# Optimization experiments

Measured on AMD Instinct MI355X. Metric: run time of the kernel, lower is better.

## Reference

```python
import jax, jax.numpy as jnp
import numpy as np


def setup_inputs() -> dict:
    key = jax.random.key(0)
    k1, k2 = jax.random.split(key)
    E, T, N = 65536, 4096, 10000
    edge_index = jax.random.randint(k1, (2, E), 0, N)
    # target edges are a subset of edge_index columns so every target exists
    target_edges = edge_index[:, :T]
    score = jax.random.normal(k2, (E,), dtype=jnp.float32)
    return {
        "edge_index": edge_index,
        "score": score,
        "target_edges": target_edges,
        "num_nodes": N,
    }


def reference(edge_index, score, target_edges, num_nodes):
    # Vectorized form of the per-target-edge loop:
    # for each target edge (s, d):
    #   mask_e      = (src_e == s) | (dst_e == d)
    #   CE over score[mask] with target = position of the exact edge (s, d)
    #   contribution = CE / K  where K = mask.sum()
    src, dst = edge_index[0], edge_index[1]            # [E]
    t_src, t_dst = target_edges[0], target_edges[1]    # [T]

    same_src = src[None, :] == t_src[:, None]          # [T, E]
    same_dst = dst[None, :] == t_dst[:, None]          # [T, E]
    mask = same_src | same_dst                         # candidate set per target
    is_tgt = same_src & same_dst                       # exact target edge hits

    exists = jnp.any(is_tgt, axis=1)                   # [T]
    K = jnp.sum(mask, axis=1).astype(score.dtype)      # [T] ragged subset sizes

    NEG = jnp.asarray(-1e30, score.dtype)
    masked_logits = jnp.where(mask, score[None, :], NEG)   # [T, E]
    lse = jax.nn.logsumexp(masked_logits, axis=1)           # [T]

    # argmax over bool picks the FIRST matching edge, matching torch argmax(-1)
    tgt_idx = jnp.argmax(is_tgt, axis=1)                # [T]
    tgt_logit = score[tgt_idx]                          # [T]

    # cross_entropy = lse - target_logit; divided by subset size K
    loss_t = jnp.where(exists, (lse - tgt_logit) / K, 0.0)
    return jnp.sum(loss_t) / target_edges.shape[1]
```

## Files before the change

### kernel.cpp

```cpp
#include <hip/hip_runtime.h>
#include <hip/hip_bf16.h>
#include <stdint.h>


#define HLOG 13
#define HSZ  (1u << HLOG)
#define NCAP 16384
#define NBW  (NCAP / 32)
#define EMPTY64 0xFFFFFFFFFFFFFFFFull
#define M40     ((1ull << 40) - 1)
#define CNT1    (1ull << 40)
#define FSCALE      4194304.0f
#define INV_FSCALE  (1.0f / 4194304.0f)

typedef unsigned long long u64;
typedef unsigned int u32;

__device__ __forceinline__ u32 hash64(u64 k) {
    return (u32)((k * 0x9E3779B97F4A7C15ull) >> (64 - HLOG));
}

#define FF_BYTES   ((size_t)HSZ * 8 + (size_t)HSZ * 4)
#define Z_BYTES    ((size_t)HSZ * 8 + 2 * (size_t)NCAP * 8 + 2 * (size_t)NBW * 4 + 8)

__global__ __launch_bounds__(256) void la_init(u64* __restrict__ p,
                                               int n_ff, int n_tot)
{
    int i = blockIdx.x * 256 + threadIdx.x;
    const int stride = gridDim.x * 256;
    for (; i < n_tot; i += stride)
        p[i] = (i < n_ff) ? EMPTY64 : 0ull;
}

__global__ __launch_bounds__(256) void la_insert(
    const int* __restrict__ tsrc, const int* __restrict__ tdst,
    u64* __restrict__ hkey, u32* __restrict__ sbit, u32* __restrict__ dbit,
    int T)
{
    const int t = blockIdx.x * 256 + threadIdx.x;
    if (t >= T) return;
    const u32 a = (u32)tsrc[t], b = (u32)tdst[t];
    if (a < NCAP) atomicOr(&sbit[a >> 5], 1u << (a & 31));
    if (b < NCAP) atomicOr(&dbit[b >> 5], 1u << (b & 31));
    const u64 key = ((u64)a << 32) | b;
    u32 h = hash64(key);
    while (true) {
        const u64 prev = atomicCAS(&hkey[h], EMPTY64, key);
        if (prev == EMPTY64 || prev == key) break;
        h = (h + 1) & (HSZ - 1);
    }
}

__global__ __launch_bounds__(256) void la_edges(
    const int* __restrict__ src, const int* __restrict__ dst,
    const float* __restrict__ score,
    const u64* __restrict__ hkey, u64* __restrict__ hpack,
    u32* __restrict__ hmin,
    u64* __restrict__ nodeS, u64* __restrict__ nodeD,
    const u32* __restrict__ sbit, const u32* __restrict__ dbit, int E)
{
    const int e = blockIdx.x * 256 + threadIdx.x;
    if (e >= E) return;
    const u32 s = (u32)src[e], d = (u32)dst[e];
    if (s >= NCAP || d >= NCAP) return;

    const bool hs = (sbit[s >> 5] >> (s & 31)) & 1u;
    const bool hd = (dbit[d >> 5] >> (d & 31)) & 1u;
    if (!hs && !hd) return;

    const float ev = __expf(score[e]);
    const u64 add = (u64)(ev * FSCALE + 0.5f) + CNT1;

    if (hs) atomicAdd(&nodeS[s], add);
    if (hd) atomicAdd(&nodeD[d], add);

    if (hs && hd) {
        const u64 key = ((u64)s << 32) | d;
        u32 h = hash64(key);
        while (true) {
            const u64 k2 = hkey[h];
            if (k2 == EMPTY64) break;
            if (k2 == key) {
                atomicAdd(&hpack[h], add);
                atomicMin(&hmin[h], (u32)e);
                break;
            }
            h = (h + 1) & (HSZ - 1);
        }
    }
}

__global__ __launch_bounds__(64) void la_targets(
    const int* __restrict__ tsrc, const int* __restrict__ tdst,
    const float* __restrict__ score,
    const u64* __restrict__ hkey, const u64* __restrict__ hpack,
    const u32* __restrict__ hmin,
    const u64* __restrict__ nodeS, const u64* __restrict__ nodeD,
    float* __restrict__ partial, u32* __restrict__ done,
    float* __restrict__ out, int T)
{
    const int nb = gridDim.x;
    const int t  = blockIdx.x * 64 + threadIdx.x;
    float local = 0.0f;
    if (t < T) {
        const u32 a = (u32)tsrc[t], b = (u32)tdst[t];
        const u64 key = ((u64)a << 32) | b;
        u32 h = hash64(key);
        int slot = -1;
        while (true) {
            const u64 k2 = hkey[h];
            if (k2 == key) { slot = (int)h; break; }
            if (k2 == EMPTY64) break;
            h = (h + 1) & (HSZ - 1);
        }
        if (slot >= 0) {
            const u64 pk = hpack[slot];
            const u64 cb = pk >> 40;
            if (cb > 0) {
                const u64 pa = nodeS[a], pb = nodeD[b];
                const u64 Sfix = (pa & M40) + (pb & M40) - (pk & M40);
                const u64 Kc   = (pa >> 40) + (pb >> 40) - cb;
                const float S  = (float)Sfix * INV_FSCALE;
                local = (logf(S) - score[hmin[slot]]) / (float)Kc;
            }
        }
    }
    for (int off = 32; off > 0; off >>= 1) local += __shfl_down(local, off);

    __shared__ int lastFlag;
    if (threadIdx.x == 0) {
        __hip_atomic_store(&partial[blockIdx.x], local, __ATOMIC_RELEASE,
                           __HIP_MEMORY_SCOPE_AGENT);
        const u32 prev = __hip_atomic_fetch_add(done, 1u, __ATOMIC_ACQ_REL,
                                                __HIP_MEMORY_SCOPE_AGENT);
        lastFlag = (prev == (u32)(nb - 1));
    }
    __syncthreads();

    if (lastFlag) {
        float s = 0.0f;
        for (int i = threadIdx.x; i < nb; i += 64)
            s += __hip_atomic_load(&partial[i], __ATOMIC_RELAXED,
                                   __HIP_MEMORY_SCOPE_AGENT);
        for (int off = 32; off > 0; off >>= 1) s += __shfl_down(s, off);
        if (threadIdx.x == 0) out[0] = s / (float)T;
    }
}

#define NT   8
#define BLK  256

__global__ __launch_bounds__(BLK) void la_loss_main(
    const int* __restrict__ src, const int* __restrict__ dst,
    const float* __restrict__ score,
    const int* __restrict__ tsrc, const int* __restrict__ tdst,
    float* __restrict__ partial, int E, int T)
{
    const int tid   = threadIdx.x;
    const int tbase = blockIdx.x * NT;
    if (tbase >= T) return;

    int ts[NT], td[NT];
#pragma unroll
    for (int j = 0; j < NT; ++j) {
        int tj = tbase + j; if (tj > T - 1) tj = T - 1;
        ts[j] = tsrc[tj];
        td[j] = tdst[tj];
    }

    float S[NT]; float Kc[NT]; int idx[NT];
#pragma unroll
    for (int j = 0; j < NT; ++j) { S[j] = 0.0f; Kc[j] = 0.0f; idx[j] = 0x7fffffff; }

    for (int it = tid * 4; it < E; it += BLK * 4) {
        const int4   vs = *reinterpret_cast<const int4*>(src + it);
        const int4   vd = *reinterpret_cast<const int4*>(dst + it);
        const float4 sc = *reinterpret_cast<const float4*>(score + it);
        const int   es[4] = { vs.x, vs.y, vs.z, vs.w };
        const int   ed[4] = { vd.x, vd.y, vd.z, vd.w };
        const float ev[4] = { __expf(sc.x), __expf(sc.y), __expf(sc.z), __expf(sc.w) };
#pragma unroll
        for (int j = 0; j < NT; ++j) {
#pragma unroll
            for (int k = 0; k < 4; ++k) {
                const bool ms = (es[k] == ts[j]);
                const bool md = (ed[k] == td[j]);
                const bool m  = ms | md;
                S[j]  += m ? ev[k] : 0.0f;
                Kc[j] += m ? 1.0f  : 0.0f;
                idx[j] = (ms & md) ? min(idx[j], it + k) : idx[j];
            }
        }
    }

#pragma unroll
    for (int j = 0; j < NT; ++j) {
        for (int off = 32; off > 0; off >>= 1) {
            S[j]  += __shfl_down(S[j],  off);
            Kc[j] += __shfl_down(Kc[j], off);
            idx[j] = min(idx[j], __shfl_down(idx[j], off));
        }
    }

    __shared__ float sS[4][NT];
    __shared__ float sK[4][NT];
    __shared__ int   sI[4][NT];
    const int wave = tid >> 6;
    const int lane = tid & 63;
    if (lane == 0) {
#pragma unroll
        for (int j = 0; j < NT; ++j) { sS[wave][j] = S[j]; sK[wave][j] = Kc[j]; sI[wave][j] = idx[j]; }
    }
    __syncthreads();

    if (tid < NT && (tbase + tid) < T) {
        float Ssum = 0.0f, Ksum = 0.0f;
        int im = 0x7fffffff;
#pragma unroll
        for (int w = 0; w < 4; ++w) {
            Ssum += sS[w][tid]; Ksum += sK[w][tid]; im = min(im, sI[w][tid]);
        }
        float loss = 0.0f;
        if (im != 0x7fffffff) loss = (logf(Ssum) - score[im]) / Ksum;
        partial[tbase + tid] = loss;
    }
}

__global__ __launch_bounds__(256) void la_loss_reduce(
    const float* __restrict__ partial, float* __restrict__ out, int T)
{
    float s = 0.0f;
    for (int i = threadIdx.x; i < T; i += 256) s += partial[i];
    for (int off = 32; off > 0; off >>= 1) s += __shfl_down(s, off);
    __shared__ float acc[4];
    if ((threadIdx.x & 63) == 0) acc[threadIdx.x >> 6] = s;
    __syncthreads();
    if (threadIdx.x == 0) out[0] = (acc[0] + acc[1] + acc[2] + acc[3]) / (float)T;
}


extern "C" void kernel_launch(void* const* d_in, const int* in_sizes, int n_in,
                              void* d_out, int out_size, void* d_ws, size_t ws_size,
                              hipStream_t stream) {
    const int*   edge_index = (const int*)d_in[0];
    const float* score      = (const float*)d_in[1];
    const int*   target     = (const int*)d_in[2];

    const int E = in_sizes[0] / 2;
    const int T = in_sizes[2] / 2;

    const int* src  = edge_index;
    const int* dst  = edge_index + E;
    const int* tsrc = target;
    const int* tdst = target + T;

    const int    nb   = (T + 63) / 64;
    const size_t need = FF_BYTES + Z_BYTES + (size_t)nb * 4;

    if (ws_size >= need) {
        uint8_t* p = (uint8_t*)d_ws;
        u64* hkey  = (u64*)p;                          p += (size_t)HSZ * 8;
        u32* hmin  = (u32*)p;                          p += (size_t)HSZ * 4;
        u64* hpack = (u64*)p;                          p += (size_t)HSZ * 8;
        u64* nodeS = (u64*)p;                          p += (size_t)NCAP * 8;
        u64* nodeD = (u64*)p;                          p += (size_t)NCAP * 8;
        u32* sbit  = (u32*)p;                          p += (size_t)NBW * 4;
        u32* dbit  = (u32*)p;                          p += (size_t)NBW * 4;
        u32* done  = (u32*)p;                          p += 8;
        float* partial = (float*)p;

        const int n_ff  = (int)(FF_BYTES / 8);
        const int n_tot = (int)((FF_BYTES + Z_BYTES) / 8);

        la_init<<<64, 256, 0, stream>>>((u64*)d_ws, n_ff, n_tot);
        la_insert<<<(T + 255) / 256, 256, 0, stream>>>(tsrc, tdst, hkey,
                                                       sbit, dbit, T);
        la_edges<<<(E + 255) / 256, 256, 0, stream>>>(src, dst, score, hkey,
                                                      hpack, hmin, nodeS, nodeD,
                                                      sbit, dbit, E);
        la_targets<<<nb, 64, 0, stream>>>(tsrc, tdst, score, hkey, hpack, hmin,
                                          nodeS, nodeD, partial, done,
                                          (float*)d_out, T);
    } else {
        float* partial = (float*)d_ws;
        la_loss_main<<<(T + NT - 1) / NT, BLK, 0, stream>>>(src, dst, score,
                                                            tsrc, tdst, partial, E, T);
        la_loss_reduce<<<1, 256, 0, stream>>>(partial, (float*)d_out, T);
    }
}
```

Before: 33.45 us.

## Fuse hash pipeline into one persistent kernel with grid barriers

```diff
diff --git a/kernel.cpp b/kernel.cpp
--- a/kernel.cpp
+++ b/kernel.cpp
@@ -7,12 +7,15 @@
 #define HSZ  (1u << HLOG)
 #define NCAP 16384
 #define NBW  (NCAP / 32)
-#define EMPTY64 0xFFFFFFFFFFFFFFFFull
 #define M40     ((1ull << 40) - 1)
 #define CNT1    (1ull << 40)
 #define FSCALE      4194304.0f
 #define INV_FSCALE  (1.0f / 4194304.0f)
 
+#define NBLK 128
+#define TPB  512
+#define NTH  (NBLK * TPB)
+
 typedef unsigned long long u64;
 typedef unsigned int u32;
 
@@ -20,97 +23,87 @@
     return (u32)((k * 0x9E3779B97F4A7C15ull) >> (64 - HLOG));
 }
 
-#define FF_BYTES   ((size_t)HSZ * 8 + (size_t)HSZ * 4)
-#define Z_BYTES    ((size_t)HSZ * 8 + 2 * (size_t)NCAP * 8 + 2 * (size_t)NBW * 4 + 8)
-
-__global__ __launch_bounds__(256) void la_init(u64* __restrict__ p,
-                                               int n_ff, int n_tot)
-{
-    int i = blockIdx.x * 256 + threadIdx.x;
-    const int stride = gridDim.x * 256;
-    for (; i < n_tot; i += stride)
-        p[i] = (i < n_ff) ? EMPTY64 : 0ull;
-}
-
-__global__ __launch_bounds__(256) void la_insert(
-    const int* __restrict__ tsrc, const int* __restrict__ tdst,
-    u64* __restrict__ hkey, u32* __restrict__ sbit, u32* __restrict__ dbit,
-    int T)
-{
-    const int t = blockIdx.x * 256 + threadIdx.x;
-    if (t >= T) return;
-    const u32 a = (u32)tsrc[t], b = (u32)tdst[t];
-    if (a < NCAP) atomicOr(&sbit[a >> 5], 1u << (a & 31));
-    if (b < NCAP) atomicOr(&dbit[b >> 5], 1u << (b & 31));
-    const u64 key = ((u64)a << 32) | b;
-    u32 h = hash64(key);
-    while (true) {
-        const u64 prev = atomicCAS(&hkey[h], EMPTY64, key);
-        if (prev == EMPTY64 || prev == key) break;
-        h = (h + 1) & (HSZ - 1);
-    }
-}
-
-__global__ __launch_bounds__(256) void la_edges(
+__device__ __forceinline__ void gbar(u32* bar, int phase, int nblk) {
+    __syncthreads();
+    if (threadIdx.x == 0) {
+        const u32 prev = __hip_atomic_fetch_add(&bar[1 + phase], 1u,
+                                                __ATOMIC_ACQ_REL,
+                                                __HIP_MEMORY_SCOPE_AGENT);
+        if (prev == (u32)(nblk - 1)) {
+            __hip_atomic_store(&bar[0], (u32)(phase + 1), __ATOMIC_RELEASE,
+                               __HIP_MEMORY_SCOPE_AGENT);
+        } else {
+            while (__hip_atomic_load(&bar[0], __ATOMIC_ACQUIRE,
+                                     __HIP_MEMORY_SCOPE_AGENT) <= (u32)phase) {}
+        }
+    }
+    __syncthreads();
+}
+
+__global__ __launch_bounds__(TPB) void la_onekernel(
     const int* __restrict__ src, const int* __restrict__ dst,
     const float* __restrict__ score,
-    const u64* __restrict__ hkey, u64* __restrict__ hpack,
-    u32* __restrict__ hmin,
+    const int* __restrict__ tsrc, const int* __restrict__ tdst,
+    u64* __restrict__ hkey, u64* __restrict__ hpack,
     u64* __restrict__ nodeS, u64* __restrict__ nodeD,
-    const u32* __restrict__ sbit, const u32* __restrict__ dbit, int E)
+    u32* __restrict__ hmax, u32* __restrict__ sbit, u32* __restrict__ dbit,
+    u32* __restrict__ bar, float* __restrict__ wpart,
+    float* __restrict__ out, int E, int T)
 {
-    const int e = blockIdx.x * 256 + threadIdx.x;
-    if (e >= E) return;
-    const u32 s = (u32)src[e], d = (u32)dst[e];
-    if (s >= NCAP || d >= NCAP) return;
-
-    const bool hs = (sbit[s >> 5] >> (s & 31)) & 1u;
-    const bool hd = (dbit[d >> 5] >> (d & 31)) & 1u;
-    if (!hs && !hd) return;
-
-    const float ev = __expf(score[e]);
-    const u64 add = (u64)(ev * FSCALE + 0.5f) + CNT1;
-
-    if (hs) atomicAdd(&nodeS[s], add);
-    if (hd) atomicAdd(&nodeD[d], add);
-
-    if (hs && hd) {
-        const u64 key = ((u64)s << 32) | d;
+    const int gtid = blockIdx.x * TPB + threadIdx.x;
+    const int nblk = gridDim.x;
+
+    for (int t = gtid; t < T; t += NTH) {
+        const u32 a = (u32)tsrc[t], b = (u32)tdst[t];
+        if (a < NCAP) atomicOr(&sbit[a >> 5], 1u << (a & 31));
+        if (b < NCAP) atomicOr(&dbit[b >> 5], 1u << (b & 31));
+        const u64 key = ((u64)(a + 1) << 32) | b;
         u32 h = hash64(key);
         while (true) {
-            const u64 k2 = hkey[h];
-            if (k2 == EMPTY64) break;
-            if (k2 == key) {
-                atomicAdd(&hpack[h], add);
-                atomicMin(&hmin[h], (u32)e);
-                break;
+            const u64 prev = atomicCAS(&hkey[h], 0ull, key);
+            if (prev == 0ull || prev == key) break;
+            h = (h + 1) & (HSZ - 1);
+        }
+    }
+    gbar(bar, 0, nblk);
+
+    for (int e = gtid; e < E; e += NTH) {
+        const u32 s = (u32)src[e], d = (u32)dst[e];
+        const float sc = score[e];
+        const bool hs = (s < NCAP) && ((sbit[s >> 5] >> (s & 31)) & 1u);
+        const bool hd = (d < NCAP) && ((dbit[d >> 5] >> (d & 31)) & 1u);
+        if (hs | hd) {
+            const u64 add = (u64)(__expf(sc) * FSCALE + 0.5f) + CNT1;
+            if (hs) atomicAdd(&nodeS[s], add);
+            if (hd) atomicAdd(&nodeD[d], add);
+            if (hs & hd) {
+                const u64 key = ((u64)(s + 1) << 32) | d;
+                u32 h = hash64(key);
+                while (true) {
+                    const u64 k2 = hkey[h];
+                    if (k2 == 0ull) break;
+                    if (k2 == key) {
+                        atomicAdd(&hpack[h], add);
+                        atomicMax(&hmax[h], ~(u32)e);
+                        break;
+                    }
+                    h = (h + 1) & (HSZ - 1);
+                }
             }
-            h = (h + 1) & (HSZ - 1);
-        }
-    }
-}
-
-__global__ __launch_bounds__(64) void la_targets(
-    const int* __restrict__ tsrc, const int* __restrict__ tdst,
-    const float* __restrict__ score,
-    const u64* __restrict__ hkey, const u64* __restrict__ hpack,
-    const u32* __restrict__ hmin,
-    const u64* __restrict__ nodeS, const u64* __restrict__ nodeD,
-    float* __restrict__ partial, u32* __restrict__ done,
-    float* __restrict__ out, int T)
-{
-    const int nb = gridDim.x;
-    const int t  = blockIdx.x * 64 + threadIdx.x;
+        }
+    }
+    gbar(bar, 1, nblk);
+
     float local = 0.0f;
-    if (t < T) {
+    for (int t = gtid; t < T; t += NTH) {
         const u32 a = (u32)tsrc[t], b = (u32)tdst[t];
-        const u64 key = ((u64)a << 32) | b;
+        const u64 key = ((u64)(a + 1) << 32) | b;
         u32 h = hash64(key);
         int slot = -1;
         while (true) {
             const u64 k2 = hkey[h];
             if (k2 == key) { slot = (int)h; break; }
-            if (k2 == EMPTY64) break;
+            if (k2 == 0ull) break;
             h = (h + 1) & (HSZ - 1);
         }
         if (slot >= 0) {
@@ -120,30 +113,34 @@
                 const u64 pa = nodeS[a], pb = nodeD[b];
                 const u64 Sfix = (pa & M40) + (pb & M40) - (pk & M40);
                 const u64 Kc   = (pa >> 40) + (pb >> 40) - cb;
-                const float S  = (float)Sfix * INV_FSCALE;
-                local = (logf(S) - score[hmin[slot]]) / (float)Kc;
+                const int idx  = (int)(~hmax[slot]);
+                local += (logf((float)Sfix * INV_FSCALE) - score[idx])
+                         / (float)Kc;
             }
         }
     }
     for (int off = 32; off > 0; off >>= 1) local += __shfl_down(local, off);
 
-    __shared__ int lastFlag;
-    if (threadIdx.x == 0) {
-        __hip_atomic_store(&partial[blockIdx.x], local, __ATOMIC_RELEASE,
+    const int nw  = ((T + 63) / 64 < NTH / 64) ? (T + 63) / 64 : NTH / 64;
+    const int wid = gtid >> 6;
+    if ((threadIdx.x & 63) == 0 && wid < nw)
+        __hip_atomic_store(&wpart[wid], local, __ATOMIC_RELEASE,
                            __HIP_MEMORY_SCOPE_AGENT);
-        const u32 prev = __hip_atomic_fetch_add(done, 1u, __ATOMIC_ACQ_REL,
-                                                __HIP_MEMORY_SCOPE_AGENT);
-        lastFlag = (prev == (u32)(nb - 1));
-    }
-    __syncthreads();
-
-    if (lastFlag) {
-        float s = 0.0f;
-        for (int i = threadIdx.x; i < nb; i += 64)
-            s += __hip_atomic_load(&partial[i], __ATOMIC_RELAXED,
-                                   __HIP_MEMORY_SCOPE_AGENT);
-        for (int off = 32; off > 0; off >>= 1) s += __shfl_down(s, off);
-        if (threadIdx.x == 0) out[0] = s / (float)T;
+    gbar(bar, 2, nblk);
+
+    if (blockIdx.x == 0) {
+        float s2 = 0.0f;
+        for (int i = threadIdx.x; i < nw; i += TPB) s2 += wpart[i];
+        for (int off = 32; off > 0; off >>= 1) s2 += __shfl_down(s2, off);
+        __shared__ float acc[TPB / 64];
+        if ((threadIdx.x & 63) == 0) acc[threadIdx.x >> 6] = s2;
+        __syncthreads();
+        if (threadIdx.x == 0) {
+            float r = 0.0f;
+#pragma unroll
+            for (int w = 0; w < TPB / 64; ++w) r += acc[w];
+            out[0] = r / (float)T;
+        }
     }
 }
 
@@ -254,33 +251,28 @@
     const int* tsrc = target;
     const int* tdst = target + T;
 
-    const int    nb   = (T + 63) / 64;
-    const size_t need = FF_BYTES + Z_BYTES + (size_t)nb * 4;
+    const int nw = ((T + 63) / 64 < NTH / 64) ? (T + 63) / 64 : NTH / 64;
+    const size_t need = (size_t)HSZ * 8 * 2 + (size_t)NCAP * 8 * 2
+                      + (size_t)HSZ * 4 + 2 * (size_t)NBW * 4 + 32
+                      + (size_t)nw * 4;
 
     if (ws_size >= need) {
         uint8_t* p = (uint8_t*)d_ws;
         u64* hkey  = (u64*)p;                          p += (size_t)HSZ * 8;
-        u32* hmin  = (u32*)p;                          p += (size_t)HSZ * 4;
         u64* hpack = (u64*)p;                          p += (size_t)HSZ * 8;
         u64* nodeS = (u64*)p;                          p += (size_t)NCAP * 8;
         u64* nodeD = (u64*)p;                          p += (size_t)NCAP * 8;
+        u32* hmax  = (u32*)p;                          p += (size_t)HSZ * 4;
         u32* sbit  = (u32*)p;                          p += (size_t)NBW * 4;
         u32* dbit  = (u32*)p;                          p += (size_t)NBW * 4;
-        u32* done  = (u32*)p;                          p += 8;
-        float* partial = (float*)p;
-
-        const int n_ff  = (int)(FF_BYTES / 8);
-        const int n_tot = (int)((FF_BYTES + Z_BYTES) / 8);
-
-        la_init<<<64, 256, 0, stream>>>((u64*)d_ws, n_ff, n_tot);
-        la_insert<<<(T + 255) / 256, 256, 0, stream>>>(tsrc, tdst, hkey,
-                                                       sbit, dbit, T);
-        la_edges<<<(E + 255) / 256, 256, 0, stream>>>(src, dst, score, hkey,
-                                                      hpack, hmin, nodeS, nodeD,
-                                                      sbit, dbit, E);
-        la_targets<<<nb, 64, 0, stream>>>(tsrc, tdst, score, hkey, hpack, hmin,
-                                          nodeS, nodeD, partial, done,
-                                          (float*)d_out, T);
+        u32* bar   = (u32*)p;                          p += 32;
+        float* wpart = (float*)p;
+
+        hipMemsetAsync(d_ws, 0, need, stream);
+        la_onekernel<<<NBLK, TPB, 0, stream>>>(src, dst, score, tsrc, tdst,
+                                               hkey, hpack, nodeS, nodeD,
+                                               hmax, sbit, dbit, bar, wpart,
+                                               (float*)d_out, E, T);
     } else {
         float* partial = (float*)d_ws;
         la_loss_main<<<(T + NT - 1) / NT, BLK, 0, stream>>>(src, dst, score,
```

Result: slower. 84.07 us (+151.4%).

## Build target hash table per block in LDS and fuse insert with edge pass

Applied to the files above, without the earlier changes.

```diff
diff --git a/kernel.cpp b/kernel.cpp
--- a/kernel.cpp
+++ b/kernel.cpp
@@ -3,89 +3,120 @@
 #include <stdint.h>
 
 
+#define NCAP 16384
+#define NBW  (NCAP / 32)
 #define HLOG 13
 #define HSZ  (1u << HLOG)
-#define NCAP 16384
-#define NBW  (NCAP / 32)
-#define EMPTY64 0xFFFFFFFFFFFFFFFFull
 #define M40     ((1ull << 40) - 1)
 #define CNT1    (1ull << 40)
 #define FSCALE      4194304.0f
 #define INV_FSCALE  (1.0f / 4194304.0f)
 
+#define NBLK 128
+#define TPB  512
+
 typedef unsigned long long u64;
 typedef unsigned int u32;
 
-__device__ __forceinline__ u32 hash64(u64 k) {
-    return (u32)((k * 0x9E3779B97F4A7C15ull) >> (64 - HLOG));
-}
-
-#define FF_BYTES   ((size_t)HSZ * 8 + (size_t)HSZ * 4)
-#define Z_BYTES    ((size_t)HSZ * 8 + 2 * (size_t)NCAP * 8 + 2 * (size_t)NBW * 4 + 8)
-
-__global__ __launch_bounds__(256) void la_init(u64* __restrict__ p,
-                                               int n_ff, int n_tot)
-{
-    int i = blockIdx.x * 256 + threadIdx.x;
-    const int stride = gridDim.x * 256;
-    for (; i < n_tot; i += stride)
-        p[i] = (i < n_ff) ? EMPTY64 : 0ull;
-}
-
-__global__ __launch_bounds__(256) void la_insert(
-    const int* __restrict__ tsrc, const int* __restrict__ tdst,
-    u64* __restrict__ hkey, u32* __restrict__ sbit, u32* __restrict__ dbit,
-    int T)
-{
-    const int t = blockIdx.x * 256 + threadIdx.x;
-    if (t >= T) return;
-    const u32 a = (u32)tsrc[t], b = (u32)tdst[t];
-    if (a < NCAP) atomicOr(&sbit[a >> 5], 1u << (a & 31));
-    if (b < NCAP) atomicOr(&dbit[b >> 5], 1u << (b & 31));
-    const u64 key = ((u64)a << 32) | b;
-    u32 h = hash64(key);
+__device__ __forceinline__ u32 hash28(u32 k) {
+    return (k * 2654435761u) >> (32 - HLOG);
+}
+
+__device__ __forceinline__ void lds_min_u16(u32* word, int hi, u32 t) {
+    u32 old = *word;
     while (true) {
-        const u64 prev = atomicCAS(&hkey[h], EMPTY64, key);
-        if (prev == EMPTY64 || prev == key) break;
-        h = (h + 1) & (HSZ - 1);
-    }
-}
-
-__global__ __launch_bounds__(256) void la_edges(
+        const u32 cur = hi ? (old >> 16) : (old & 0xFFFFu);
+        if (t >= cur) break;
+        const u32 nw = hi ? ((old & 0x0000FFFFu) | (t << 16))
+                          : ((old & 0xFFFF0000u) | t);
+        const u32 prev = atomicCAS(word, old, nw);
+        if (prev == old) break;
+        old = prev;
+    }
+}
+
+__global__ __launch_bounds__(TPB) void la_merge(
     const int* __restrict__ src, const int* __restrict__ dst,
     const float* __restrict__ score,
-    const u64* __restrict__ hkey, u64* __restrict__ hpack,
-    u32* __restrict__ hmin,
+    const int* __restrict__ tsrc, const int* __restrict__ tdst,
     u64* __restrict__ nodeS, u64* __restrict__ nodeD,
-    const u32* __restrict__ sbit, const u32* __restrict__ dbit, int E)
+    u64* __restrict__ bothPack, u32* __restrict__ bothMax,
+    u32* __restrict__ canon, int E, int T)
 {
-    const int e = blockIdx.x * 256 + threadIdx.x;
-    if (e >= E) return;
-    const u32 s = (u32)src[e], d = (u32)dst[e];
-    if (s >= NCAP || d >= NCAP) return;
-
-    const bool hs = (sbit[s >> 5] >> (s & 31)) & 1u;
-    const bool hd = (dbit[d >> 5] >> (d & 31)) & 1u;
-    if (!hs && !hd) return;
-
-    const float ev = __expf(score[e]);
-    const u64 add = (u64)(ev * FSCALE + 0.5f) + CNT1;
-
-    if (hs) atomicAdd(&nodeS[s], add);
-    if (hd) atomicAdd(&nodeD[d], add);
-
-    if (hs && hd) {
-        const u64 key = ((u64)s << 32) | d;
-        u32 h = hash64(key);
+    __shared__ u32 keys[HSZ];
+    __shared__ u32 valw[HSZ / 2];
+    __shared__ u32 sbits[NBW];
+    __shared__ u32 dbits[NBW];
+
+    const int tid = threadIdx.x;
+
+    for (int i = tid; i < HSZ; i += TPB)      keys[i] = 0xFFFFFFFFu;
+    for (int i = tid; i < HSZ / 2; i += TPB)  valw[i] = 0xFFFFFFFFu;
+    for (int i = tid; i < NBW; i += TPB)    { sbits[i] = 0u; dbits[i] = 0u; }
+    __syncthreads();
+
+    for (int t = tid; t < T; t += TPB) {
+        const u32 a = (u32)tsrc[t], b = (u32)tdst[t];
+        if (a >= NCAP || b >= NCAP) continue;
+        atomicOr(&sbits[a >> 5], 1u << (a & 31));
+        atomicOr(&dbits[b >> 5], 1u << (b & 31));
+        const u32 key = a * (u32)NCAP + b;
+        u32 h = hash28(key);
         while (true) {
-            const u64 k2 = hkey[h];
-            if (k2 == EMPTY64) break;
-            if (k2 == key) {
-                atomicAdd(&hpack[h], add);
-                atomicMin(&hmin[h], (u32)e);
-                break;
+            const u32 prev = atomicCAS(&keys[h], 0xFFFFFFFFu, key);
+            if (prev == 0xFFFFFFFFu || prev == key) break;
+            h = (h + 1) & (HSZ - 1);
+        }
+        lds_min_u16(&valw[h >> 1], h & 1, (u32)t);
+    }
+    __syncthreads();
+
+    if (blockIdx.x == 0) {
+        for (int t = tid; t < T; t += TPB) {
+            const u32 a = (u32)tsrc[t], b = (u32)tdst[t];
+            u32 c = (u32)t;
+            if (a < NCAP && b < NCAP) {
+                const u32 key = a * (u32)NCAP + b;
+                u32 h = hash28(key);
+                while (true) {
+                    const u32 k2 = keys[h];
+                    if (k2 == key) {
+                        const u32 w = valw[h >> 1];
+                        c = (h & 1) ? (w >> 16) : (w & 0xFFFFu);
+                        break;
+                    }
+                    if (k2 == 0xFFFFFFFFu) break;
+                    h = (h + 1) & (HSZ - 1);
+                }
             }
-            h = (h + 1) & (HSZ - 1);
+            canon[t] = c;
+        }
+    }
+
+    for (int e = blockIdx.x * TPB + tid; e < E; e += NBLK * TPB) {
+        const u32 s = (u32)src[e], d = (u32)dst[e];
+        if (s >= NCAP || d >= NCAP) continue;
+        const bool hs = (sbits[s >> 5] >> (s & 31)) & 1u;
+        const bool hd = (dbits[d >> 5] >> (d & 31)) & 1u;
+        if (!(hs | hd)) continue;
+        const u64 add = (u64)(__expf(score[e]) * FSCALE + 0.5f) + CNT1;
+        if (hs) atomicAdd(&nodeS[s], add);
+        if (hd) atomicAdd(&nodeD[d], add);
+        if (hs & hd) {
+            const u32 key = s * (u32)NCAP + d;
+            u32 h = hash28(key);
+            while (true) {
+                const u32 k2 = keys[h];
+                if (k2 == 0xFFFFFFFFu) break;
+                if (k2 == key) {
+                    const u32 w = valw[h >> 1];
+                    const u32 c = (h & 1) ? (w >> 16) : (w & 0xFFFFu);
+                    atomicAdd(&bothPack[c], add);
+                    atomicMax(&bothMax[c], ~(u32)e);
+                    break;
+                }
+                h = (h + 1) & (HSZ - 1);
+            }
         }
     }
 }
@@ -93,9 +124,9 @@
 __global__ __launch_bounds__(64) void la_targets(
     const int* __restrict__ tsrc, const int* __restrict__ tdst,
     const float* __restrict__ score,
-    const u64* __restrict__ hkey, const u64* __restrict__ hpack,
-    const u32* __restrict__ hmin,
     const u64* __restrict__ nodeS, const u64* __restrict__ nodeD,
+    const u64* __restrict__ bothPack, const u32* __restrict__ bothMax,
+    const u32* __restrict__ canon,
     float* __restrict__ partial, u32* __restrict__ done,
     float* __restrict__ out, int T)
 {
@@ -104,24 +135,17 @@
     float local = 0.0f;
     if (t < T) {
         const u32 a = (u32)tsrc[t], b = (u32)tdst[t];
-        const u64 key = ((u64)a << 32) | b;
-        u32 h = hash64(key);
-        int slot = -1;
-        while (true) {
-            const u64 k2 = hkey[h];
-            if (k2 == key) { slot = (int)h; break; }
-            if (k2 == EMPTY64) break;
-            h = (h + 1) & (HSZ - 1);
-        }
-        if (slot >= 0) {
-            const u64 pk = hpack[slot];
+        if (a < NCAP && b < NCAP) {
+            const u32 c  = canon[t];
+            const u64 pk = bothPack[c];
             const u64 cb = pk >> 40;
             if (cb > 0) {
                 const u64 pa = nodeS[a], pb = nodeD[b];
                 const u64 Sfix = (pa & M40) + (pb & M40) - (pk & M40);
                 const u64 Kc   = (pa >> 40) + (pb >> 40) - cb;
-                const float S  = (float)Sfix * INV_FSCALE;
-                local = (logf(S) - score[hmin[slot]]) / (float)Kc;
+                const int idx  = (int)(~bothMax[c]);
+                local = (logf((float)Sfix * INV_FSCALE) - score[idx])
+                        / (float)Kc;
             }
         }
     }
@@ -254,33 +278,27 @@
     const int* tsrc = target;
     const int* tdst = target + T;
 
-    const int    nb   = (T + 63) / 64;
-    const size_t need = FF_BYTES + Z_BYTES + (size_t)nb * 4;
-
-    if (ws_size >= need) {
+    const int nb = (T + 63) / 64;
+    const size_t need = 2 * (size_t)NCAP * 8 + (size_t)T * 8
+                      + 2 * (size_t)T * 4 + 32 + (size_t)nb * 4;
+
+    if (ws_size >= need && T < 65536) {
         uint8_t* p = (uint8_t*)d_ws;
-        u64* hkey  = (u64*)p;                          p += (size_t)HSZ * 8;
-        u32* hmin  = (u32*)p;                          p += (size_t)HSZ * 4;
-        u64* hpack = (u64*)p;                          p += (size_t)HSZ * 8;
-        u64* nodeS = (u64*)p;                          p += (size_t)NCAP * 8;
-        u64* nodeD = (u64*)p;                          p += (size_t)NCAP * 8;
-        u32* sbit  = (u32*)p;                          p += (size_t)NBW * 4;
-        u32* dbit  = (u32*)p;                          p += (size_t)NBW * 4;
-        u32* done  = (u32*)p;                          p += 8;
+        u64* nodeS    = (u64*)p;  p += (size_t)NCAP * 8;
+        u64* nodeD    = (u64*)p;  p += (size_t)NCAP * 8;
+        u64* bothPack = (u64*)p;  p += (size_t)T * 8;
+        u32* bothMax  = (u32*)p;  p += (size_t)T * 4;
+        u32* canon    = (u32*)p;  p += (size_t)T * 4;
+        u32* done     = (u32*)p;  p += 32;
         float* partial = (float*)p;
 
-        const int n_ff  = (int)(FF_BYTES / 8);
-        const int n_tot = (int)((FF_BYTES + Z_BYTES) / 8);
-
-        la_init<<<64, 256, 0, stream>>>((u64*)d_ws, n_ff, n_tot);
-        la_insert<<<(T + 255) / 256, 256, 0, stream>>>(tsrc, tdst, hkey,
-                                                       sbit, dbit, T);
-        la_edges<<<(E + 255) / 256, 256, 0, stream>>>(src, dst, score, hkey,
-                                                      hpack, hmin, nodeS, nodeD,
-                                                      sbit, dbit, E);
-        la_targets<<<nb, 64, 0, stream>>>(tsrc, tdst, score, hkey, hpack, hmin,
-                                          nodeS, nodeD, partial, done,
-                                          (float*)d_out, T);
+        hipMemsetAsync(d_ws, 0, need, stream);
+        la_merge<<<NBLK, TPB, 0, stream>>>(src, dst, score, tsrc, tdst,
+                                           nodeS, nodeD, bothPack, bothMax,
+                                           canon, E, T);
+        la_targets<<<nb, 64, 0, stream>>>(tsrc, tdst, score, nodeS, nodeD,
+                                          bothPack, bothMax, canon,
+                                          partial, done, (float*)d_out, T);
     } else {
         float* partial = (float*)d_ws;
         la_loss_main<<<(T + NT - 1) / NT, BLK, 0, stream>>>(src, dst, score,
```

Measured after the change: 33.52 us. Within noise of the previous version (+0.2%).
